# Optimization experiments

Hardware: AMD Instinct MI355X
Metric: run time of the kernel (lower is better)

## Reference

```python
import jax, jax.numpy as jnp
import numpy as np

TEMPERATURE = 0.07
IGNORE_INDEX = 255
MAX_SAMPLES = 1024  # K
BACKGROUND = 0
EPS = 1e-8


def setup_inputs() -> dict:
    key = jax.random.key(0)
    k1, k2 = jax.random.split(key)
    B, C, H, W = 16, 256, 128, 128
    feats = jax.random.normal(k1, (B, C, H, W), dtype=jnp.float32)
    labels = jax.random.randint(k2, (B, H, W), 0, 4).astype(jnp.int64)
    return {"feats": feats, "labels": labels}


def _sample_pixels(feats_flat, labels_flat, K):
    """Deterministic analogue of the torch sampler: positives first, then
    background negatives, invalid last (original uses randperm; the math
    downstream is identical for any such selection). Pads exactly like the
    original: zero features, ignore_index labels, boolean valid mask."""
    # priority: 0 = foreground pos, 1 = background neg, 2 = ignore
    prio = jnp.where(labels_flat == IGNORE_INDEX, 2,
                     jnp.where(labels_flat == BACKGROUND, 1, 0))
    order = jnp.argsort(prio, axis=1)[:, :K]                      # [B, K] stable sort
    sel_prio = jnp.take_along_axis(prio, order, axis=1)
    valid = sel_prio < 2                                          # [B, K] bool
    s_feats = jnp.take_along_axis(feats_flat, order[:, :, None], axis=1)
    s_feats = s_feats * valid[:, :, None].astype(s_feats.dtype)   # zero-pad like F.pad
    s_labels = jnp.where(valid, jnp.take_along_axis(labels_flat, order, axis=1),
                         IGNORE_INDEX)
    return s_feats, s_labels, valid


def reference(feats, labels):
    B, C, H, W = feats.shape
    K = MAX_SAMPLES
    f = feats.transpose(0, 2, 3, 1).reshape(B, H * W, C)          # [B, N, C]
    l = labels.reshape(B, H * W)

    s_feats, s_labels, valid = _sample_pixels(f, l, K)

    # pair each image with the next (rolled) image -> [B, 2K, .]
    fp = jnp.concatenate([s_feats, jnp.roll(s_feats, -1, axis=0)], axis=1)
    lp = jnp.concatenate([s_labels, jnp.roll(s_labels, -1, axis=0)], axis=1)
    vp = jnp.concatenate([valid, jnp.roll(valid, -1, axis=0)], axis=1)

    # F.normalize(dim=2), eps=1e-12
    fp = fp / jnp.maximum(jnp.linalg.norm(fp, axis=2, keepdims=True), 1e-12)

    vf = vp.astype(fp.dtype)
    logits = jnp.einsum('bkc,bjc->bkj', fp, fp) / TEMPERATURE      # [B, 2K, 2K]
    logits = logits - jax.lax.stop_gradient(jnp.max(logits, axis=2, keepdims=True))

    v_matrix = vf[:, :, None] * vf[:, None, :]
    pos_mask = (lp[:, :, None] == lp[:, None, :]).astype(fp.dtype) * v_matrix
    same_img = jnp.kron(jnp.eye(2, dtype=fp.dtype), jnp.ones((K, K), dtype=fp.dtype))[None]
    neg_mask = (1.0 - pos_mask) * same_img * v_matrix
    not_self = 1.0 - jnp.eye(2 * K, dtype=fp.dtype)[None]
    pos_mask = pos_mask * not_self
    neg_mask = neg_mask * not_self

    exp_logits = jnp.exp(logits)
    sum_neg = jnp.sum(exp_logits * neg_mask, axis=2, keepdims=True)
    log_probs = logits - jnp.log(exp_logits + sum_neg + EPS)

    num_pos = jnp.maximum(pos_mask.sum(axis=2), 1.0)
    mean_log_prob = (pos_mask * log_probs).sum(axis=2) / num_pos
    valid_anchors = (pos_mask.sum(axis=2) > 0).astype(fp.dtype)
    loss_img = (-mean_log_prob * valid_anchors).sum(axis=1) / jnp.maximum(
        valid_anchors.sum(axis=1), 1.0)                            # [B]

    # with valid labels everywhere, every chunk is valid -> divide by B
    return loss_img.sum() / B
```

## Files before the change

### kernel.cpp

```cpp
#include <hip/hip_runtime.h>
#include <hip/hip_bf16.h>

namespace {

constexpr int NB  = 16;
constexpr int NC  = 256;
constexpr int NHW = 16384;
constexpr int NK  = 1024;
constexpr int IGN = 255;
constexpr float SCALE = 4.5398164f;
constexpr float CBIAS = 20.609929f;
constexpr float LN2   = 0.69314718f;

typedef __attribute__((ext_vector_type(8))) short short8;
typedef __attribute__((ext_vector_type(4))) float f32x4;
typedef unsigned int u32;

#define ASM_VMCNT8 asm volatile("s_waitcnt vmcnt(8)" ::: "memory")
#define ASM_VMCNT0 asm volatile("s_waitcnt vmcnt(0)" ::: "memory")
#define ASM_LGKM0  asm volatile("s_waitcnt lgkmcnt(0)" ::: "memory")
#define SCHEDB     __builtin_amdgcn_sched_barrier(0)
#define MEMFENCE   asm volatile("" ::: "memory")
#define BARRIER    __builtin_amdgcn_s_barrier()
#define ACQ_AGENT  __builtin_amdgcn_fence(__ATOMIC_ACQUIRE, "agent")

__device__ __forceinline__ float fexp2(float x) { return __builtin_exp2f(x); }

__device__ __forceinline__ void gl_lds16(const void* g, void* l) {
  __builtin_amdgcn_global_load_lds((const __attribute__((address_space(1))) u32*)g,
                                   (__attribute__((address_space(3))) u32*)l, 16, 0, 0);
}

__global__ __launch_bounds__(1024) void pcl_sample(const int* __restrict__ labels,
                                                   int* __restrict__ sel_lab,
                                                   int* __restrict__ sel_idx,
                                                   int* __restrict__ cnt,
                                                   int* __restrict__ findone) {
  const int b = blockIdx.x, t = threadIdx.x, lane = t & 63, w = t >> 6;
  if (t == 0) { cnt[b] = 0; if (b == 0) *findone = 0; }
  __shared__ int labL[1024 * 17];
  __shared__ int wtot[16];

  sel_lab[b * NK + t] = IGN;

  const int* lab = labels + b * NHW;
#pragma unroll
  for (int k = 0; k < 16; ++k) {
    int idx = k * 1024 + t;
    labL[(idx >> 4) * 17 + (idx & 15)] = lab[idx];
  }
  __syncthreads();

  int cfg = 0, cbg = 0;
#pragma unroll
  for (int i = 0; i < 16; ++i) {
    int L = labL[t * 17 + i];
    cfg += (L != IGN && L != 0);
    cbg += (L == 0);
  }
  int packed = cfg | (cbg << 15);
  int incl = packed;
#pragma unroll
  for (int off = 1; off < 64; off <<= 1) {
    int n = __shfl_up(incl, off);
    if (lane >= off) incl += n;
  }
  if (lane == 63) wtot[w] = incl;
  __syncthreads();
  int wb = 0, total = 0;
#pragma unroll
  for (int ww = 0; ww < 16; ++ww) { int v = wtot[ww]; total += v; if (ww < w) wb += v; }
  int excl = incl - packed + wb;
  int rf  = excl & 32767;
  int rbg = (excl >> 15) & 32767;
  const int nfg = total & 32767;
  if (rf < NK || nfg + rbg < NK) {
#pragma unroll
    for (int i = 0; i < 16; ++i) {
      int L = labL[t * 17 + i];
      if (L == IGN) continue;
      if (L != 0) {
        if (rf < NK) { sel_lab[b * NK + rf] = L; sel_idx[b * NK + rf] = t * 16 + i; }
        ++rf;
      } else {
        int s = nfg + rbg;
        if (s < NK) { sel_lab[b * NK + s] = L; sel_idx[b * NK + s] = t * 16 + i; }
        ++rbg;
      }
    }
  }
}

__global__ __launch_bounds__(1024) void pcl_gather(const float* __restrict__ feats,
                                                   const int* __restrict__ sel_lab,
                                                   const int* __restrict__ sel_idx,
                                                   unsigned short* __restrict__ SF) {
  const int b = blockIdx.x >> 4, kb = blockIdx.x & 15;
  const int t = threadIdx.x, s = t & 63, w = t >> 6;
  __shared__ float fbuf[64][257];
  __shared__ float sqs[16][64];
  __shared__ float rn[64];
  const int gk = b * NK + kb * 64 + s;
  const int lb = sel_lab[gk];
  const int p = (lb != IGN) ? sel_idx[gk] : -1;
  const float* fb = feats + (size_t)b * NC * NHW;
  float sq = 0.f;
#pragma unroll
  for (int cc = 0; cc < 16; ++cc) {
    int c = w * 16 + cc;
    float v = (p >= 0) ? fb[(size_t)c * NHW + p] : 0.f;
    fbuf[s][c] = v;
    sq += v * v;
  }
  sqs[w][s] = sq;
  __syncthreads();
  if (t < 64) {
    float tot = 0.f;
#pragma unroll
    for (int k2 = 0; k2 < 16; ++k2) tot += sqs[k2][t];
    rn[t] = SCALE / fmaxf(sqrtf(tot), 1e-12f);
  }
  __syncthreads();
#pragma unroll
  for (int it = 0; it < 2; ++it) {
    int slot = it * 1024 + t;
    int ss = slot >> 5, ch = slot & 31;
    float r = rn[ss];
    short8 v8;
#pragma unroll
    for (int e = 0; e < 8; ++e) {
      float x = fbuf[ss][ch * 8 + e] * r;
      __hip_bfloat16 h = __float2bfloat16(x);
      unsigned short u; __builtin_memcpy(&u, &h, 2);
      v8[e] = (short)u;
    }
    *(short8*)(SF + ((size_t)(b * NK + kb * 64 + ss)) * NC + ch * 8) = v8;
  }
}

__global__ __launch_bounds__(512) void pcl_tiles(
    const unsigned short* __restrict__ SF, const int* __restrict__ sel_lab,
    float2* __restrict__ SNd, float4* __restrict__ Rii, float4* __restrict__ Cp,
    float2* __restrict__ A1arr, float2* __restrict__ Aimg,
    int* __restrict__ cnt, int* __restrict__ findone, float* __restrict__ out) {
  const int id = blockIdx.x;
  const int i = id & 15, strip = id >> 4;
  const int inxt = (i + 1) & 15, iprev = (i + 15) & 15;
  const int t = threadIdx.x, lane = t & 63, w = t >> 6;
  const int rw = w & 1, ch4 = w >> 1;
  const int lg = lane >> 4, lr = lane & 15;
  const float SFAC = __builtin_exp2f(-CBIAS);

  __shared__ short buf[2][128 * 256];
  __shared__ float4 colAcc[2][128];
  __shared__ float4 rredS[4][64];
  __shared__ float4 rredX[4][64];
  __shared__ float2 fold2[8];
  __shared__ int fA, fB;

  const unsigned short* SFrow = SF + (size_t)i * (NK * NC) + strip * 64 * NC;

  auto stage_round = [&](int rr) {
    const unsigned short* base =
        SF + (size_t)((rr < 8) ? i : inxt) * (NK * NC) + ((rr & 7) * 128) * NC;
    short* dst = buf[rr & 1];
#pragma unroll
    for (int it = 0; it < 8; ++it) {
      int n = it * 512 + t, row = n >> 5, ch = n & 31;
      gl_lds16(base + row * NC + ((ch ^ (row & 15)) << 3), dst + (size_t)n * 8);
    }
  };

#pragma unroll
  for (int it = 0; it < 4; ++it) {
    int n = it * 512 + t, row = n >> 5, ch = n & 31;
    gl_lds16(SFrow + row * NC + ((ch ^ (row & 15)) << 3), buf[0] + (size_t)n * 8);
  }
  ASM_VMCNT0; MEMFENCE; BARRIER; MEMFENCE;

  short8 afrag[2][8];
#pragma unroll
  for (int rt = 0; rt < 2; ++rt) {
    const int arow = rw * 32 + rt * 16 + lr;
#pragma unroll
    for (int ks = 0; ks < 8; ++ks) {
      int ch = ks * 4 + lg;
      afrag[rt][ks] = *(const short8*)(buf[0] + arow * 256 + ((ch ^ (arow & 15)) << 3));
    }
  }
  ASM_LGKM0; SCHEDB; MEMFENCE; BARRIER; MEMFENCE;

  stage_round(0);
  stage_round(1);

  int rlab[2][4];
#pragma unroll
  for (int rt = 0; rt < 2; ++rt)
#pragma unroll
    for (int jj = 0; jj < 4; ++jj) {
      int L = sel_lab[i * NK + strip * 64 + rw * 32 + rt * 16 + 4 * lg + jj];
      rlab[rt][jj] = (L == IGN) ? -1 : L;
    }

  ASM_VMCNT8; MEMFENCE; BARRIER; MEMFENCE;

  float SA[2][4], NPr[2][4], PEr[2][4], ETr[2][4];
#pragma unroll
  for (int rt = 0; rt < 2; ++rt)
#pragma unroll
    for (int jj = 0; jj < 4; ++jj) { SA[rt][jj] = 0.f; NPr[rt][jj] = 0.f; PEr[rt][jj] = 0.f; ETr[rt][jj] = 0.f; }

  const int rs = strip >> 1;
  const bool dwave = ((ch4 >> 1) == (strip & 1));

  for (int r = 0; r < 8; ++r) {
    int cl[2]; float cvf[2];
#pragma unroll
    for (int c2 = 0; c2 < 2; ++c2) {
      int L = sel_lab[i * NK + r * 128 + ch4 * 32 + c2 * 16 + lr];
      cl[c2] = (L == IGN) ? -2 : L;
      cvf[c2] = (L == IGN) ? 0.f : 1.f;
    }

    const short* bb = buf[r & 1];
    f32x4 acc[2][2];
#pragma unroll
    for (int rt = 0; rt < 2; ++rt)
#pragma unroll
      for (int c2 = 0; c2 < 2; ++c2) acc[rt][c2] = f32x4{0.f, 0.f, 0.f, 0.f};
#pragma unroll
    for (int ks = 0; ks < 8; ++ks) {
      int ch = ks * 4 + lg;
      short8 b0, b1;
      {
        int br0 = ch4 * 32 + lr, br1 = ch4 * 32 + 16 + lr;
        b0 = *(const short8*)(bb + br0 * 256 + ((ch ^ (br0 & 15)) << 3));
        b1 = *(const short8*)(bb + br1 * 256 + ((ch ^ (br1 & 15)) << 3));
      }
      acc[0][0] = __builtin_amdgcn_mfma_f32_16x16x32_bf16(afrag[0][ks], b0, acc[0][0], 0, 0, 0);
      acc[0][1] = __builtin_amdgcn_mfma_f32_16x16x32_bf16(afrag[0][ks], b1, acc[0][1], 0, 0, 0);
      acc[1][0] = __builtin_amdgcn_mfma_f32_16x16x32_bf16(afrag[1][ks], b0, acc[1][0], 0, 0, 0);
      acc[1][1] = __builtin_amdgcn_mfma_f32_16x16x32_bf16(afrag[1][ks], b1, acc[1][1], 0, 0, 0);
    }

    const bool isdiag = (r == rs) && dwave;
#pragma unroll
    for (int rt = 0; rt < 2; ++rt)
#pragma unroll
      for (int c2 = 0; c2 < 2; ++c2) {
        const int clc = cl[c2]; const float cvc = cvf[c2];
        const int gc = r * 128 + ch4 * 32 + c2 * 16 + lr;
        const int grb = strip * 64 + rw * 32 + rt * 16 + 4 * lg;
#pragma unroll
        for (int jj = 0; jj < 4; ++jj) {
          float a = acc[rt][c2][jj];
          float E = fexp2(a);
          float Ev = cvc * E;
          float pm = (rlab[rt][jj] == clc) ? 1.f : 0.f;
          if (isdiag) {
            bool ok = (grb + jj) != gc;
            pm = ok ? pm : 0.f;
            Ev = ok ? Ev : 0.f;
          }
          SA[rt][jj] += pm * a; NPr[rt][jj] += pm;
          PEr[rt][jj] += pm * Ev; ETr[rt][jj] += Ev;
        }
      }

    MEMFENCE; BARRIER; MEMFENCE;
    stage_round(r + 2);
    ASM_VMCNT8;
    MEMFENCE; BARRIER; MEMFENCE;
  }

#pragma unroll
  for (int rt = 0; rt < 2; ++rt)
#pragma unroll
    for (int jj = 0; jj < 4; ++jj) {
      float a = SA[rt][jj], b4 = NPr[rt][jj], c4 = PEr[rt][jj], d4 = ETr[rt][jj];
#pragma unroll
      for (int m = 1; m <= 8; m <<= 1) {
        a += __shfl_xor(a, m); b4 += __shfl_xor(b4, m);
        c4 += __shfl_xor(c4, m); d4 += __shfl_xor(d4, m);
      }
      if (lr == 0) rredS[ch4][rw * 32 + rt * 16 + 4 * lg + jj] = make_float4(a, b4, c4, d4);
    }

  float SX[2][4], NX[2][4], PX[2][4];
#pragma unroll
  for (int rt = 0; rt < 2; ++rt)
#pragma unroll
    for (int jj = 0; jj < 4; ++jj) { SX[rt][jj] = 0.f; NX[rt][jj] = 0.f; PX[rt][jj] = 0.f; }

  for (int r = 8; r < 16; ++r) {
    int cl[2];
#pragma unroll
    for (int c2 = 0; c2 < 2; ++c2) {
      int L = sel_lab[inxt * NK + (r & 7) * 128 + ch4 * 32 + c2 * 16 + lr];
      cl[c2] = (L == IGN) ? -2 : L;
    }

    const short* bb = buf[r & 1];
    f32x4 acc[2][2];
#pragma unroll
    for (int rt = 0; rt < 2; ++rt)
#pragma unroll
      for (int c2 = 0; c2 < 2; ++c2) acc[rt][c2] = f32x4{0.f, 0.f, 0.f, 0.f};
#pragma unroll
    for (int ks = 0; ks < 8; ++ks) {
      int ch = ks * 4 + lg;
      short8 b0, b1;
      {
        int br0 = ch4 * 32 + lr, br1 = ch4 * 32 + 16 + lr;
        b0 = *(const short8*)(bb + br0 * 256 + ((ch ^ (br0 & 15)) << 3));
        b1 = *(const short8*)(bb + br1 * 256 + ((ch ^ (br1 & 15)) << 3));
      }
      acc[0][0] = __builtin_amdgcn_mfma_f32_16x16x32_bf16(afrag[0][ks], b0, acc[0][0], 0, 0, 0);
      acc[0][1] = __builtin_amdgcn_mfma_f32_16x16x32_bf16(afrag[0][ks], b1, acc[0][1], 0, 0, 0);
      acc[1][0] = __builtin_amdgcn_mfma_f32_16x16x32_bf16(afrag[1][ks], b0, acc[1][0], 0, 0, 0);
      acc[1][1] = __builtin_amdgcn_mfma_f32_16x16x32_bf16(afrag[1][ks], b1, acc[1][1], 0, 0, 0);
    }

    float cS[2], cN[2], cE[2];
#pragma unroll
    for (int c2 = 0; c2 < 2; ++c2) { cS[c2] = 0.f; cN[c2] = 0.f; cE[c2] = 0.f; }
#pragma unroll
    for (int rt = 0; rt < 2; ++rt)
#pragma unroll
      for (int c2 = 0; c2 < 2; ++c2) {
        const int clc = cl[c2];
#pragma unroll
        for (int jj = 0; jj < 4; ++jj) {
          float a = acc[rt][c2][jj];
          float E = fexp2(a);
          float pm = (rlab[rt][jj] == clc) ? 1.f : 0.f;
          float pa = pm * a, pe = pm * E;
          SX[rt][jj] += pa; NX[rt][jj] += pm; PX[rt][jj] += pe;
          cS[c2] += pa; cN[c2] += pm; cE[c2] += pe;
        }
      }
#pragma unroll
    for (int c2 = 0; c2 < 2; ++c2) {
      cS[c2] += __shfl_xor(cS[c2], 16); cS[c2] += __shfl_xor(cS[c2], 32);
      cN[c2] += __shfl_xor(cN[c2], 16); cN[c2] += __shfl_xor(cN[c2], 32);
      cE[c2] += __shfl_xor(cE[c2], 16); cE[c2] += __shfl_xor(cE[c2], 32);
      if (lg == 0) colAcc[rw][ch4 * 32 + c2 * 16 + lr] = make_float4(cS[c2], cN[c2], cE[c2], 0.f);
    }
    ASM_LGKM0; SCHEDB;
    MEMFENCE; BARRIER; MEMFENCE;
    if (rw == 1 && lg == 0) {
#pragma unroll
      for (int c2 = 0; c2 < 2; ++c2) {
        int col = ch4 * 32 + c2 * 16 + lr;
        float4 o = colAcc[0][col];
        Cp[(i * 16 + strip) * NK + (r & 7) * 128 + col] =
            make_float4(cS[c2] + o.x, cN[c2] + o.y, (cE[c2] + o.z) * SFAC, 0.f);
      }
    }
    if (r < 14) { stage_round(r + 2); ASM_VMCNT8; MEMFENCE; BARRIER; MEMFENCE; }
    else if (r == 14) { ASM_VMCNT0; MEMFENCE; BARRIER; MEMFENCE; }
  }

#pragma unroll
  for (int rt = 0; rt < 2; ++rt)
#pragma unroll
    for (int jj = 0; jj < 4; ++jj) {
      float a = SX[rt][jj], b4 = NX[rt][jj], c4 = PX[rt][jj];
#pragma unroll
      for (int m = 1; m <= 8; m <<= 1) {
        a += __shfl_xor(a, m); b4 += __shfl_xor(b4, m); c4 += __shfl_xor(c4, m);
      }
      if (lr == 0) rredX[ch4][rw * 32 + rt * 16 + 4 * lg + jj] = make_float4(a, b4, c4, 0.f);
    }
  __syncthreads();

  if (t < 64) {
    float4 sS = rredS[0][t], sX = rredX[0][t];
#pragma unroll
    for (int c4 = 1; c4 < 4; ++c4) {
      float4 u = rredS[c4][t], v = rredX[c4][t];
      sS.x += u.x; sS.y += u.y; sS.z += u.z; sS.w += u.w;
      sX.x += v.x; sX.y += v.y; sX.z += v.z;
    }
    float SNL = sS.w - sS.z;
    float SN = SNL * SFAC + 1e-8f;
    float LSN = __logf(SN), rSN = 1.f / SN;
    int g = i * NK + strip * 64 + t;
    SNd[g] = make_float2(LSN, rSN);
    Rii[g] = make_float4(sS.x, sS.y, sS.z * SFAC, 0.f);
    float pps = LN2 * (sS.x - CBIAS * sS.y) - sS.y * LSN - rSN * (sS.z * SFAC);
    float ppx = LN2 * (sX.x - CBIAS * sX.y) - sX.y * LSN - rSN * (sX.z * SFAC);
    float np1 = sS.y + sX.y;
    float an = 0.f, ac = 0.f;
    if (np1 > 0.f) { an = -(pps + ppx) / np1; ac = 1.f; }
#pragma unroll
    for (int m = 1; m <= 32; m <<= 1) { an += __shfl_xor(an, m); ac += __shfl_xor(ac, m); }
    if (t == 0) A1arr[i * 16 + strip] = make_float2(an, ac);
  }
  __syncthreads();

  if (t == 0) {
    __threadfence();
    int o1 = atomicAdd(&cnt[i], 1);
    int o2 = atomicAdd(&cnt[iprev], 1);
    fA = (o1 == 31); fB = (o2 == 31);
  }
  __syncthreads();

  auto pair_fold = [&](int p) {
    const int q = (p + 1) & 15;
    ACQ_AGENT;
    float an = 0.f, ac = 0.f;
    for (int r2 = t; r2 < NK; r2 += 512) {
      float4 rii = Rii[q * NK + r2];
      float2 sn = SNd[q * NK + r2];
      float cs = 0.f, cn = 0.f, ce = 0.f;
#pragma unroll
      for (int s2 = 0; s2 < 16; ++s2) {
        float4 c = Cp[(p * 16 + s2) * NK + r2];
        cs += c.x; cn += c.y; ce += c.z;
      }
      float ppc = LN2 * (cs - CBIAS * cn) - cn * sn.x - sn.y * ce;
      float ppi = LN2 * (rii.x - CBIAS * rii.y) - rii.y * sn.x - sn.y * rii.z;
      float np2 = rii.y + cn;
      if (np2 > 0.f) { an -= (ppi + ppc) / np2; ac += 1.f; }
    }
#pragma unroll
    for (int m = 1; m <= 32; m <<= 1) { an += __shfl_xor(an, m); ac += __shfl_xor(ac, m); }
    if (lane == 0) fold2[w] = make_float2(an, ac);
    __syncthreads();
    if (t == 0) {
      float a2n = 0.f, a2c = 0.f;
#pragma unroll
      for (int k2 = 0; k2 < 8; ++k2) { a2n += fold2[k2].x; a2c += fold2[k2].y; }
      float a1n = 0.f, a1c = 0.f;
#pragma unroll
      for (int s2 = 0; s2 < 16; ++s2) {
        float2 a = A1arr[q * 16 + s2];
        a1n += a.x; a1c += a.y;
      }
      Aimg[q] = make_float2(a1n + a2n, a1c + a2c);
      __threadfence();
      int f = atomicAdd(findone, 1);
      if (f == NB - 1) {
        ACQ_AGENT;
        float v = 0.f;
#pragma unroll
        for (int im = 0; im < NB; ++im) {
          float2 gg = Aimg[im];
          v += gg.x / fmaxf(gg.y, 1.f);
        }
        out[0] = v / (float)NB;
      }
    }
    __syncthreads();
  };

  if (fA) pair_fold(i);
  if (fB) pair_fold(iprev);
}

}

extern "C" void kernel_launch(void* const* d_in, const int* in_sizes, int n_in,
                              void* d_out, int out_size, void* d_ws, size_t ws_size,
                              hipStream_t stream) {
  (void)in_sizes; (void)n_in; (void)out_size; (void)ws_size;
  const float* feats  = (const float*)d_in[0];
  const int*   labels = (const int*)d_in[1];
  float* out = (float*)d_out;
  char* ws = (char*)d_ws;

  int* sel_lab = (int*)ws;
  int* sel_idx = (int*)(ws + (64 << 10));
  unsigned short* SF = (unsigned short*)(ws + (128 << 10));
  size_t off = (128 << 10) + (size_t)NB * NK * NC * 2;
  float2* SNd = (float2*)(ws + off);  off += (size_t)NB * NK * 8;
  float4* Rii = (float4*)(ws + off);  off += (size_t)NB * NK * 16;
  float4* Cp  = (float4*)(ws + off);  off += (size_t)NB * 16 * NK * 16;
  float2* A1arr = (float2*)(ws + off); off += (size_t)NB * 16 * 8;
  float2* Aimg = (float2*)(ws + off);  off += NB * 8;
  int* cnt = (int*)(ws + off);         off += 16 * 4;
  int* findone = (int*)(ws + off);

  pcl_sample<<<NB, 1024, 0, stream>>>(labels, sel_lab, sel_idx, cnt, findone);
  pcl_gather<<<256, 1024, 0, stream>>>(feats, sel_lab, sel_idx, SF);
  pcl_tiles<<<256, 512, 0, stream>>>(SF, sel_lab, SNd, Rii, Cp, A1arr, Aimg,
                                     cnt, findone, out);
}
```

Baseline: 87.61 us.

## Fuse sampling, gather and tile kernels into one kernel with a spin barrier

Merges the three launches (label sampling, feature gather with normalisation, similarity tiles) into a single 256-block kernel, with the shared-memory layouts overlaid in a union. Each block recomputes the label prefix scan for its own image and keeps only its 64-slot strip locally, so the separate sel_idx buffer goes away. A per-image ready counter, zeroed by a memset, plus a spin-wait lets a block start its tile work once its own image and the next image are gathered. This removes inter-kernel launch gaps and the 16-block serial sampling stage. The cost is 16x redundant label scans, redundant identical writes to sel_lab, and a deadlock risk if all 256 blocks cannot be resident at once.

```diff
diff --git a/kernel.cpp b/kernel.cpp
--- a/kernel.cpp
+++ b/kernel.cpp
@@ -31,139 +31,157 @@
                                    (__attribute__((address_space(3))) u32*)l, 16, 0, 0);
 }
 
-__global__ __launch_bounds__(1024) void pcl_sample(const int* __restrict__ labels,
-                                                   int* __restrict__ sel_lab,
-                                                   int* __restrict__ sel_idx,
-                                                   int* __restrict__ cnt,
-                                                   int* __restrict__ findone) {
-  const int b = blockIdx.x, t = threadIdx.x, lane = t & 63, w = t >> 6;
-  if (t == 0) { cnt[b] = 0; if (b == 0) *findone = 0; }
-  __shared__ int labL[1024 * 17];
-  __shared__ int wtot[16];
-
-  sel_lab[b * NK + t] = IGN;
-
-  const int* lab = labels + b * NHW;
-#pragma unroll
-  for (int k = 0; k < 16; ++k) {
-    int idx = k * 1024 + t;
-    labL[(idx >> 4) * 17 + (idx & 15)] = lab[idx];
-  }
-  __syncthreads();
-
-  int cfg = 0, cbg = 0;
-#pragma unroll
-  for (int i = 0; i < 16; ++i) {
-    int L = labL[t * 17 + i];
-    cfg += (L != IGN && L != 0);
-    cbg += (L == 0);
-  }
-  int packed = cfg | (cbg << 15);
-  int incl = packed;
-#pragma unroll
-  for (int off = 1; off < 64; off <<= 1) {
-    int n = __shfl_up(incl, off);
-    if (lane >= off) incl += n;
-  }
-  if (lane == 63) wtot[w] = incl;
-  __syncthreads();
-  int wb = 0, total = 0;
-#pragma unroll
-  for (int ww = 0; ww < 16; ++ww) { int v = wtot[ww]; total += v; if (ww < w) wb += v; }
-  int excl = incl - packed + wb;
-  int rf  = excl & 32767;
-  int rbg = (excl >> 15) & 32767;
-  const int nfg = total & 32767;
-  if (rf < NK || nfg + rbg < NK) {
-#pragma unroll
-    for (int i = 0; i < 16; ++i) {
-      int L = labL[t * 17 + i];
-      if (L == IGN) continue;
-      if (L != 0) {
-        if (rf < NK) { sel_lab[b * NK + rf] = L; sel_idx[b * NK + rf] = t * 16 + i; }
-        ++rf;
-      } else {
-        int s = nfg + rbg;
-        if (s < NK) { sel_lab[b * NK + s] = L; sel_idx[b * NK + s] = t * 16 + i; }
-        ++rbg;
-      }
-    }
-  }
-}
-
-__global__ __launch_bounds__(1024) void pcl_gather(const float* __restrict__ feats,
-                                                   const int* __restrict__ sel_lab,
-                                                   const int* __restrict__ sel_idx,
-                                                   unsigned short* __restrict__ SF) {
-  const int b = blockIdx.x >> 4, kb = blockIdx.x & 15;
-  const int t = threadIdx.x, s = t & 63, w = t >> 6;
-  __shared__ float fbuf[64][257];
-  __shared__ float sqs[16][64];
-  __shared__ float rn[64];
-  const int gk = b * NK + kb * 64 + s;
-  const int lb = sel_lab[gk];
-  const int p = (lb != IGN) ? sel_idx[gk] : -1;
-  const float* fb = feats + (size_t)b * NC * NHW;
-  float sq = 0.f;
-#pragma unroll
-  for (int cc = 0; cc < 16; ++cc) {
-    int c = w * 16 + cc;
-    float v = (p >= 0) ? fb[(size_t)c * NHW + p] : 0.f;
-    fbuf[s][c] = v;
-    sq += v * v;
-  }
-  sqs[w][s] = sq;
-  __syncthreads();
-  if (t < 64) {
-    float tot = 0.f;
-#pragma unroll
-    for (int k2 = 0; k2 < 16; ++k2) tot += sqs[k2][t];
-    rn[t] = SCALE / fmaxf(sqrtf(tot), 1e-12f);
-  }
-  __syncthreads();
-#pragma unroll
-  for (int it = 0; it < 2; ++it) {
-    int slot = it * 1024 + t;
-    int ss = slot >> 5, ch = slot & 31;
-    float r = rn[ss];
-    short8 v8;
-#pragma unroll
-    for (int e = 0; e < 8; ++e) {
-      float x = fbuf[ss][ch * 8 + e] * r;
-      __hip_bfloat16 h = __float2bfloat16(x);
-      unsigned short u; __builtin_memcpy(&u, &h, 2);
-      v8[e] = (short)u;
-    }
-    *(short8*)(SF + ((size_t)(b * NK + kb * 64 + ss)) * NC + ch * 8) = v8;
-  }
-}
-
-__global__ __launch_bounds__(512) void pcl_tiles(
-    const unsigned short* __restrict__ SF, const int* __restrict__ sel_lab,
+union SmemU {
+  struct {
+    int lab[NHW + (NHW >> 5)];
+    int wtot[8];
+  } s;
+  struct {
+    float fbuf[64][257];
+    float sqs[8][64];
+    float rn[64];
+  } g;
+  struct {
+    short buf[2][128 * 256];
+    float4 colAcc[2][128];
+    float4 rredS[4][64];
+    float4 rredX[4][64];
+    float2 fold2[8];
+    int fA, fB;
+  } t3;
+};
+
+__global__ __launch_bounds__(512) void pcl_fused(
+    const int* __restrict__ labels, const float* __restrict__ feats,
+    int* __restrict__ sel_lab, unsigned short* __restrict__ SF,
     float2* __restrict__ SNd, float4* __restrict__ Rii, float4* __restrict__ Cp,
     float2* __restrict__ A1arr, float2* __restrict__ Aimg,
-    int* __restrict__ cnt, int* __restrict__ findone, float* __restrict__ out) {
+    int* __restrict__ cnt, int* __restrict__ gready, int* __restrict__ findone,
+    float* __restrict__ out) {
   const int id = blockIdx.x;
   const int i = id & 15, strip = id >> 4;
   const int inxt = (i + 1) & 15, iprev = (i + 15) & 15;
   const int t = threadIdx.x, lane = t & 63, w = t >> 6;
+
+  __shared__ SmemU sm;
+  __shared__ int slab[64], sidx[64];
+
+  {
+    const int* lab = labels + (size_t)i * NHW;
+#pragma unroll
+    for (int k = 0; k < 32; ++k) {
+      int idx = k * 512 + t;
+      sm.s.lab[idx + (idx >> 5)] = lab[idx];
+    }
+    if (t < 64) slab[t] = IGN;
+    __syncthreads();
+
+    int cfg = 0, cbg = 0;
+#pragma unroll
+    for (int j = 0; j < 32; ++j) {
+      int L = sm.s.lab[t * 33 + j];
+      cfg += (L != IGN && L != 0);
+      cbg += (L == 0);
+    }
+    int packed = cfg | (cbg << 15);
+    int incl = packed;
+#pragma unroll
+    for (int off = 1; off < 64; off <<= 1) {
+      int n = __shfl_up(incl, off);
+      if (lane >= off) incl += n;
+    }
+    if (lane == 63) sm.s.wtot[w] = incl;
+    __syncthreads();
+    int wb = 0, total = 0;
+#pragma unroll
+    for (int ww = 0; ww < 8; ++ww) { int v = sm.s.wtot[ww]; total += v; if (ww < w) wb += v; }
+    int excl = incl - packed + wb;
+    int rf  = excl & 32767;
+    int rbg = (excl >> 15) & 32767;
+    const int nfg = total & 32767;
+    const int nbg = (total >> 15) & 32767;
+    const int ncap = min(NK, nfg + nbg);
+    for (int k2 = ncap + t; k2 < NK; k2 += 512) sel_lab[i * NK + k2] = IGN;
+
+    const int s0 = strip * 64;
+    if (rf < NK || nfg + rbg < NK) {
+      for (int j = 0; j < 32; ++j) {
+        int L = sm.s.lab[t * 33 + j];
+        if (L == IGN) continue;
+        int slot;
+        if (L != 0) { slot = rf; ++rf; }
+        else        { slot = nfg + rbg; ++rbg; }
+        if (slot < NK) {
+          sel_lab[i * NK + slot] = L;
+          int d = slot - s0;
+          if ((unsigned)d < 64u) { slab[d] = L; sidx[d] = t * 32 + j; }
+        }
+      }
+    }
+    __syncthreads();
+  }
+
+  {
+    const int ss = t & 63, w8 = t >> 6;
+    const int lb = slab[ss];
+    const int p = (lb != IGN) ? sidx[ss] : -1;
+    const float* fb = feats + (size_t)i * NC * NHW;
+    float sq = 0.f;
+#pragma unroll
+    for (int cc = 0; cc < 32; ++cc) {
+      int c = w8 * 32 + cc;
+      float v = (p >= 0) ? fb[(size_t)c * NHW + p] : 0.f;
+      sm.g.fbuf[ss][c] = v;
+      sq += v * v;
+    }
+    sm.g.sqs[w8][ss] = sq;
+    __syncthreads();
+    if (t < 64) {
+      float tot = 0.f;
+#pragma unroll
+      for (int k2 = 0; k2 < 8; ++k2) tot += sm.g.sqs[k2][t];
+      sm.g.rn[t] = SCALE / fmaxf(sqrtf(tot), 1e-12f);
+    }
+    __syncthreads();
+    unsigned short* SFo = SF + ((size_t)(i * NK + strip * 64)) * NC;
+#pragma unroll
+    for (int it2 = 0; it2 < 4; ++it2) {
+      int n = it2 * 512 + t;
+      int row = n >> 5, ch16 = n & 31;
+      float r = sm.g.rn[row];
+      short8 v8;
+#pragma unroll
+      for (int e = 0; e < 8; ++e) {
+        float x = sm.g.fbuf[row][ch16 * 8 + e] * r;
+        __hip_bfloat16 h = __float2bfloat16(x);
+        unsigned short u; __builtin_memcpy(&u, &h, 2);
+        v8[e] = (short)u;
+      }
+      *(short8*)(SFo + (size_t)row * NC + ch16 * 8) = v8;
+    }
+    __syncthreads();
+
+    if (t == 0) {
+      __threadfence();
+      atomicAdd(&gready[i], 1);
+      while (__hip_atomic_load(&gready[i],    __ATOMIC_RELAXED, __HIP_MEMORY_SCOPE_AGENT) < 16 ||
+             __hip_atomic_load(&gready[inxt], __ATOMIC_RELAXED, __HIP_MEMORY_SCOPE_AGENT) < 16)
+        __builtin_amdgcn_s_sleep(2);
+      ACQ_AGENT;
+    }
+    __syncthreads();
+  }
+
   const int rw = w & 1, ch4 = w >> 1;
   const int lg = lane >> 4, lr = lane & 15;
   const float SFAC = __builtin_exp2f(-CBIAS);
 
-  __shared__ short buf[2][128 * 256];
-  __shared__ float4 colAcc[2][128];
-  __shared__ float4 rredS[4][64];
-  __shared__ float4 rredX[4][64];
-  __shared__ float2 fold2[8];
-  __shared__ int fA, fB;
-
   const unsigned short* SFrow = SF + (size_t)i * (NK * NC) + strip * 64 * NC;
 
   auto stage_round = [&](int rr) {
     const unsigned short* base =
         SF + (size_t)((rr < 8) ? i : inxt) * (NK * NC) + ((rr & 7) * 128) * NC;
-    short* dst = buf[rr & 1];
+    short* dst = sm.t3.buf[rr & 1];
 #pragma unroll
     for (int it = 0; it < 8; ++it) {
       int n = it * 512 + t, row = n >> 5, ch = n & 31;
@@ -174,7 +192,7 @@
 #pragma unroll
   for (int it = 0; it < 4; ++it) {
     int n = it * 512 + t, row = n >> 5, ch = n & 31;
-    gl_lds16(SFrow + row * NC + ((ch ^ (row & 15)) << 3), buf[0] + (size_t)n * 8);
+    gl_lds16(SFrow + row * NC + ((ch ^ (row & 15)) << 3), sm.t3.buf[0] + (size_t)n * 8);
   }
   ASM_VMCNT0; MEMFENCE; BARRIER; MEMFENCE;
 
@@ -185,7 +203,7 @@
 #pragma unroll
     for (int ks = 0; ks < 8; ++ks) {
       int ch = ks * 4 + lg;
-      afrag[rt][ks] = *(const short8*)(buf[0] + arow * 256 + ((ch ^ (arow & 15)) << 3));
+      afrag[rt][ks] = *(const short8*)(sm.t3.buf[0] + arow * 256 + ((ch ^ (arow & 15)) << 3));
     }
   }
   ASM_LGKM0; SCHEDB; MEMFENCE; BARRIER; MEMFENCE;
@@ -222,7 +240,7 @@
       cvf[c2] = (L == IGN) ? 0.f : 1.f;
     }
 
-    const short* bb = buf[r & 1];
+    const short* bb = sm.t3.buf[r & 1];
     f32x4 acc[2][2];
 #pragma unroll
     for (int rt = 0; rt < 2; ++rt)
@@ -283,7 +301,7 @@
         a += __shfl_xor(a, m); b4 += __shfl_xor(b4, m);
         c4 += __shfl_xor(c4, m); d4 += __shfl_xor(d4, m);
       }
-      if (lr == 0) rredS[ch4][rw * 32 + rt * 16 + 4 * lg + jj] = make_float4(a, b4, c4, d4);
+      if (lr == 0) sm.t3.rredS[ch4][rw * 32 + rt * 16 + 4 * lg + jj] = make_float4(a, b4, c4, d4);
     }
 
   float SX[2][4], NX[2][4], PX[2][4];
@@ -300,7 +318,7 @@
       cl[c2] = (L == IGN) ? -2 : L;
     }
 
-    const short* bb = buf[r & 1];
+    const short* bb = sm.t3.buf[r & 1];
     f32x4 acc[2][2];
 #pragma unroll
     for (int rt = 0; rt < 2; ++rt)
@@ -344,7 +362,7 @@
       cS[c2] += __shfl_xor(cS[c2], 16); cS[c2] += __shfl_xor(cS[c2], 32);
       cN[c2] += __shfl_xor(cN[c2], 16); cN[c2] += __shfl_xor(cN[c2], 32);
       cE[c2] += __shfl_xor(cE[c2], 16); cE[c2] += __shfl_xor(cE[c2], 32);
-      if (lg == 0) colAcc[rw][ch4 * 32 + c2 * 16 + lr] = make_float4(cS[c2], cN[c2], cE[c2], 0.f);
+      if (lg == 0) sm.t3.colAcc[rw][ch4 * 32 + c2 * 16 + lr] = make_float4(cS[c2], cN[c2], cE[c2], 0.f);
     }
     ASM_LGKM0; SCHEDB;
     MEMFENCE; BARRIER; MEMFENCE;
@@ -352,7 +370,7 @@
 #pragma unroll
       for (int c2 = 0; c2 < 2; ++c2) {
         int col = ch4 * 32 + c2 * 16 + lr;
-        float4 o = colAcc[0][col];
+        float4 o = sm.t3.colAcc[0][col];
         Cp[(i * 16 + strip) * NK + (r & 7) * 128 + col] =
             make_float4(cS[c2] + o.x, cN[c2] + o.y, (cE[c2] + o.z) * SFAC, 0.f);
       }
@@ -370,15 +388,15 @@
       for (int m = 1; m <= 8; m <<= 1) {
         a += __shfl_xor(a, m); b4 += __shfl_xor(b4, m); c4 += __shfl_xor(c4, m);
       }
-      if (lr == 0) rredX[ch4][rw * 32 + rt * 16 + 4 * lg + jj] = make_float4(a, b4, c4, 0.f);
+      if (lr == 0) sm.t3.rredX[ch4][rw * 32 + rt * 16 + 4 * lg + jj] = make_float4(a, b4, c4, 0.f);
     }
   __syncthreads();
 
   if (t < 64) {
-    float4 sS = rredS[0][t], sX = rredX[0][t];
+    float4 sS = sm.t3.rredS[0][t], sX = sm.t3.rredX[0][t];
 #pragma unroll
     for (int c4 = 1; c4 < 4; ++c4) {
-      float4 u = rredS[c4][t], v = rredX[c4][t];
+      float4 u = sm.t3.rredS[c4][t], v = sm.t3.rredX[c4][t];
       sS.x += u.x; sS.y += u.y; sS.z += u.z; sS.w += u.w;
       sX.x += v.x; sX.y += v.y; sX.z += v.z;
     }
@@ -403,7 +421,7 @@
     __threadfence();
     int o1 = atomicAdd(&cnt[i], 1);
     int o2 = atomicAdd(&cnt[iprev], 1);
-    fA = (o1 == 31); fB = (o2 == 31);
+    sm.t3.fA = (o1 == 31); sm.t3.fB = (o2 == 31);
   }
   __syncthreads();
 
@@ -427,12 +445,12 @@
     }
 #pragma unroll
     for (int m = 1; m <= 32; m <<= 1) { an += __shfl_xor(an, m); ac += __shfl_xor(ac, m); }
-    if (lane == 0) fold2[w] = make_float2(an, ac);
+    if (lane == 0) sm.t3.fold2[w] = make_float2(an, ac);
     __syncthreads();
     if (t == 0) {
       float a2n = 0.f, a2c = 0.f;
 #pragma unroll
-      for (int k2 = 0; k2 < 8; ++k2) { a2n += fold2[k2].x; a2c += fold2[k2].y; }
+      for (int k2 = 0; k2 < 8; ++k2) { a2n += sm.t3.fold2[k2].x; a2c += sm.t3.fold2[k2].y; }
       float a1n = 0.f, a1c = 0.f;
 #pragma unroll
       for (int s2 = 0; s2 < 16; ++s2) {
@@ -456,8 +474,8 @@
     __syncthreads();
   };
 
-  if (fA) pair_fold(i);
-  if (fB) pair_fold(iprev);
+  if (sm.t3.fA) pair_fold(i);
+  if (sm.t3.fB) pair_fold(iprev);
 }
 
 }
@@ -472,19 +490,18 @@
   char* ws = (char*)d_ws;
 
   int* sel_lab = (int*)ws;
-  int* sel_idx = (int*)(ws + (64 << 10));
-  unsigned short* SF = (unsigned short*)(ws + (128 << 10));
-  size_t off = (128 << 10) + (size_t)NB * NK * NC * 2;
+  unsigned short* SF = (unsigned short*)(ws + (64 << 10));
+  size_t off = (64 << 10) + (size_t)NB * NK * NC * 2;
   float2* SNd = (float2*)(ws + off);  off += (size_t)NB * NK * 8;
   float4* Rii = (float4*)(ws + off);  off += (size_t)NB * NK * 16;
   float4* Cp  = (float4*)(ws + off);  off += (size_t)NB * 16 * NK * 16;
   float2* A1arr = (float2*)(ws + off); off += (size_t)NB * 16 * 8;
   float2* Aimg = (float2*)(ws + off);  off += NB * 8;
-  int* cnt = (int*)(ws + off);         off += 16 * 4;
-  int* findone = (int*)(ws + off);
-
-  pcl_sample<<<NB, 1024, 0, stream>>>(labels, sel_lab, sel_idx, cnt, findone);
-  pcl_gather<<<256, 1024, 0, stream>>>(feats, sel_lab, sel_idx, SF);
-  pcl_tiles<<<256, 512, 0, stream>>>(SF, sel_lab, SNd, Rii, Cp, A1arr, Aimg,
-                                     cnt, findone, out);
+  int* cnt = (int*)(ws + off);
+  int* gready = cnt + 16;
+  int* findone = cnt + 32;
+
+  hipMemsetAsync(cnt, 0, 33 * sizeof(int), stream);
+  pcl_fused<<<256, 512, 0, stream>>>(labels, feats, sel_lab, SF, SNd, Rii, Cp,
+                                     A1arr, Aimg, cnt, gready, findone, out);
 }
```

Result: slower. 124.0 us (+41.5%).

## Split tile work into self and cross-image blocks with smaller workgroups

Applied to the files above, without the earlier changes.

The tile kernel goes from 256 blocks of 512 threads, each covering a 64-row strip against both the same image and the next image, to 512 blocks of 256 threads. Each block now handles one 64-row strip against only one column image (self or next), using 64-column staging rounds. The completion counters and the final fold are reworked to match: 48 contributors per image, separate Rin and AimgA/AimgB buffers. Block-to-image mappings in the gather and tile kernels are remapped, apparently to spread images across XCDs. The intent is more parallelism and occupancy on the 256-CU part, at the cost of reloading row fragments twice and more atomic and fold traffic.

```diff
diff --git a/kernel.cpp b/kernel.cpp
--- a/kernel.cpp
+++ b/kernel.cpp
@@ -34,10 +34,10 @@
 __global__ __launch_bounds__(1024) void pcl_sample(const int* __restrict__ labels,
                                                    int* __restrict__ sel_lab,
                                                    int* __restrict__ sel_idx,
-                                                   int* __restrict__ cnt,
+                                                   int* __restrict__ fc,
                                                    int* __restrict__ findone) {
   const int b = blockIdx.x, t = threadIdx.x, lane = t & 63, w = t >> 6;
-  if (t == 0) { cnt[b] = 0; if (b == 0) *findone = 0; }
+  if (t == 0) { fc[b] = 0; if (b == 0) *findone = 0; }
   __shared__ int labL[1024 * 17];
   __shared__ int wtot[16];
 
@@ -95,7 +95,9 @@
                                                    const int* __restrict__ sel_lab,
                                                    const int* __restrict__ sel_idx,
                                                    unsigned short* __restrict__ SF) {
-  const int b = blockIdx.x >> 4, kb = blockIdx.x & 15;
+  const int id = blockIdx.x;
+  const int b = (id & 7) + (((id >> 3) & 1) << 3);
+  const int kb = id >> 4;
   const int t = threadIdx.x, s = t & 63, w = t >> 6;
   __shared__ float fbuf[64][257];
   __shared__ float sqs[16][64];
@@ -138,42 +140,48 @@
   }
 }
 
-__global__ __launch_bounds__(512) void pcl_tiles(
+__global__ __launch_bounds__(256) void pcl_tiles(
     const unsigned short* __restrict__ SF, const int* __restrict__ sel_lab,
-    float2* __restrict__ SNd, float4* __restrict__ Rii, float4* __restrict__ Cp,
-    float2* __restrict__ A1arr, float2* __restrict__ Aimg,
-    int* __restrict__ cnt, int* __restrict__ findone, float* __restrict__ out) {
+    float2* __restrict__ SNd, float4* __restrict__ Rii, float4* __restrict__ Rin,
+    float4* __restrict__ Cp, float2* __restrict__ AimgA, float2* __restrict__ AimgB,
+    int* __restrict__ fc, int* __restrict__ findone, float* __restrict__ out) {
   const int id = blockIdx.x;
-  const int i = id & 15, strip = id >> 4;
-  const int inxt = (i + 1) & 15, iprev = (i + 15) & 15;
+  const int g = id & 7, slot = id >> 3;
+  const bool selfm = slot < 32;
+  const int strip = slot & 15;
+  int i;
+  if (selfm) i = (slot < 16) ? g : g + 8;
+  else { int j1 = (g + 7) & 7; i = (slot < 48) ? j1 : j1 + 8; }
+  const int inxt = (i + 1) & 15;
+  const int jimg = selfm ? i : inxt;
+
   const int t = threadIdx.x, lane = t & 63, w = t >> 6;
-  const int rw = w & 1, ch4 = w >> 1;
+  const int rw = w & 1, cw = w >> 1;
   const int lg = lane >> 4, lr = lane & 15;
   const float SFAC = __builtin_exp2f(-CBIAS);
 
-  __shared__ short buf[2][128 * 256];
-  __shared__ float4 colAcc[2][128];
-  __shared__ float4 rredS[4][64];
-  __shared__ float4 rredX[4][64];
-  __shared__ float2 fold2[8];
+  __shared__ short buf[2][64 * 256];
+  __shared__ float4 colAcc[2][64];
+  __shared__ float4 rred[2][64];
+  __shared__ float4 fold4[4];
   __shared__ int fA, fB;
 
   const unsigned short* SFrow = SF + (size_t)i * (NK * NC) + strip * 64 * NC;
+  const unsigned short* SFcol = SF + (size_t)jimg * (NK * NC);
 
   auto stage_round = [&](int rr) {
-    const unsigned short* base =
-        SF + (size_t)((rr < 8) ? i : inxt) * (NK * NC) + ((rr & 7) * 128) * NC;
+    const unsigned short* base = SFcol + ((rr)*64) * NC;
     short* dst = buf[rr & 1];
 #pragma unroll
     for (int it = 0; it < 8; ++it) {
-      int n = it * 512 + t, row = n >> 5, ch = n & 31;
+      int n = it * 256 + t, row = n >> 5, ch = n & 31;
       gl_lds16(base + row * NC + ((ch ^ (row & 15)) << 3), dst + (size_t)n * 8);
     }
   };
 
 #pragma unroll
-  for (int it = 0; it < 4; ++it) {
-    int n = it * 512 + t, row = n >> 5, ch = n & 31;
+  for (int it = 0; it < 8; ++it) {
+    int n = it * 256 + t, row = n >> 5, ch = n & 31;
     gl_lds16(SFrow + row * NC + ((ch ^ (row & 15)) << 3), buf[0] + (size_t)n * 8);
   }
   ASM_VMCNT0; MEMFENCE; BARRIER; MEMFENCE;
@@ -204,20 +212,17 @@
 
   ASM_VMCNT8; MEMFENCE; BARRIER; MEMFENCE;
 
-  float SA[2][4], NPr[2][4], PEr[2][4], ETr[2][4];
+  float S1[2][4], N1[2][4], P1[2][4], ET[2][4];
 #pragma unroll
   for (int rt = 0; rt < 2; ++rt)
 #pragma unroll
-    for (int jj = 0; jj < 4; ++jj) { SA[rt][jj] = 0.f; NPr[rt][jj] = 0.f; PEr[rt][jj] = 0.f; ETr[rt][jj] = 0.f; }
-
-  const int rs = strip >> 1;
-  const bool dwave = ((ch4 >> 1) == (strip & 1));
-
-  for (int r = 0; r < 8; ++r) {
+    for (int jj = 0; jj < 4; ++jj) { S1[rt][jj] = 0.f; N1[rt][jj] = 0.f; P1[rt][jj] = 0.f; ET[rt][jj] = 0.f; }
+
+  for (int r = 0; r < 16; ++r) {
     int cl[2]; float cvf[2];
 #pragma unroll
     for (int c2 = 0; c2 < 2; ++c2) {
-      int L = sel_lab[i * NK + r * 128 + ch4 * 32 + c2 * 16 + lr];
+      int L = sel_lab[jimg * NK + r * 64 + cw * 32 + c2 * 16 + lr];
       cl[c2] = (L == IGN) ? -2 : L;
       cvf[c2] = (L == IGN) ? 0.f : 1.f;
     }
@@ -233,7 +238,7 @@
       int ch = ks * 4 + lg;
       short8 b0, b1;
       {
-        int br0 = ch4 * 32 + lr, br1 = ch4 * 32 + 16 + lr;
+        int br0 = cw * 32 + lr, br1 = cw * 32 + 16 + lr;
         b0 = *(const short8*)(bb + br0 * 256 + ((ch ^ (br0 & 15)) << 3));
         b1 = *(const short8*)(bb + br1 * 256 + ((ch ^ (br1 & 15)) << 3));
       }
@@ -243,177 +248,128 @@
       acc[1][1] = __builtin_amdgcn_mfma_f32_16x16x32_bf16(afrag[1][ks], b1, acc[1][1], 0, 0, 0);
     }
 
-    const bool isdiag = (r == rs) && dwave;
-#pragma unroll
-    for (int rt = 0; rt < 2; ++rt)
+    if (selfm) {
+      const bool isdiag = (r == strip);
+#pragma unroll
+      for (int rt = 0; rt < 2; ++rt)
+#pragma unroll
+        for (int c2 = 0; c2 < 2; ++c2) {
+          const int clc = cl[c2]; const float cvc = cvf[c2];
+          const int gc = r * 64 + cw * 32 + c2 * 16 + lr;
+          const int grb = strip * 64 + rw * 32 + rt * 16 + 4 * lg;
+#pragma unroll
+          for (int jj = 0; jj < 4; ++jj) {
+            float a = acc[rt][c2][jj];
+            float E = fexp2(a);
+            float Ev = cvc * E;
+            float pm = (rlab[rt][jj] == clc) ? 1.f : 0.f;
+            if (isdiag) {
+              bool ok = (grb + jj) != gc;
+              pm = ok ? pm : 0.f;
+              Ev = ok ? Ev : 0.f;
+            }
+            S1[rt][jj] += pm * a; N1[rt][jj] += pm;
+            P1[rt][jj] += pm * Ev; ET[rt][jj] += Ev;
+          }
+        }
+      MEMFENCE; BARRIER; MEMFENCE;
+    } else {
+      float cS[2], cN[2], cE[2];
+#pragma unroll
+      for (int c2 = 0; c2 < 2; ++c2) { cS[c2] = 0.f; cN[c2] = 0.f; cE[c2] = 0.f; }
+#pragma unroll
+      for (int rt = 0; rt < 2; ++rt)
+#pragma unroll
+        for (int c2 = 0; c2 < 2; ++c2) {
+          const int clc = cl[c2];
+#pragma unroll
+          for (int jj = 0; jj < 4; ++jj) {
+            float a = acc[rt][c2][jj];
+            float E = fexp2(a);
+            float pm = (rlab[rt][jj] == clc) ? 1.f : 0.f;
+            float pa = pm * a, pe = pm * E;
+            S1[rt][jj] += pa; N1[rt][jj] += pm; P1[rt][jj] += pe;
+            cS[c2] += pa; cN[c2] += pm; cE[c2] += pe;
+          }
+        }
 #pragma unroll
       for (int c2 = 0; c2 < 2; ++c2) {
-        const int clc = cl[c2]; const float cvc = cvf[c2];
-        const int gc = r * 128 + ch4 * 32 + c2 * 16 + lr;
-        const int grb = strip * 64 + rw * 32 + rt * 16 + 4 * lg;
-#pragma unroll
-        for (int jj = 0; jj < 4; ++jj) {
-          float a = acc[rt][c2][jj];
-          float E = fexp2(a);
-          float Ev = cvc * E;
-          float pm = (rlab[rt][jj] == clc) ? 1.f : 0.f;
-          if (isdiag) {
-            bool ok = (grb + jj) != gc;
-            pm = ok ? pm : 0.f;
-            Ev = ok ? Ev : 0.f;
-          }
-          SA[rt][jj] += pm * a; NPr[rt][jj] += pm;
-          PEr[rt][jj] += pm * Ev; ETr[rt][jj] += Ev;
+        cS[c2] += __shfl_xor(cS[c2], 16); cS[c2] += __shfl_xor(cS[c2], 32);
+        cN[c2] += __shfl_xor(cN[c2], 16); cN[c2] += __shfl_xor(cN[c2], 32);
+        cE[c2] += __shfl_xor(cE[c2], 16); cE[c2] += __shfl_xor(cE[c2], 32);
+        if (lg == 0) colAcc[rw][cw * 32 + c2 * 16 + lr] = make_float4(cS[c2], cN[c2], cE[c2], 0.f);
+      }
+      ASM_LGKM0; SCHEDB;
+      MEMFENCE; BARRIER; MEMFENCE;
+      if (rw == 1 && lg == 0) {
+#pragma unroll
+        for (int c2 = 0; c2 < 2; ++c2) {
+          int col = cw * 32 + c2 * 16 + lr;
+          float4 o = colAcc[0][col];
+          Cp[(i * 16 + strip) * NK + r * 64 + col] =
+              make_float4(cS[c2] + o.x, cN[c2] + o.y, (cE[c2] + o.z) * SFAC, 0.f);
         }
       }
-
-    MEMFENCE; BARRIER; MEMFENCE;
-    stage_round(r + 2);
-    ASM_VMCNT8;
-    MEMFENCE; BARRIER; MEMFENCE;
+    }
+
+    if (r < 14) { stage_round(r + 2); ASM_VMCNT8; MEMFENCE; BARRIER; MEMFENCE; }
+    else if (r == 14) { ASM_VMCNT0; MEMFENCE; BARRIER; MEMFENCE; }
   }
 
 #pragma unroll
   for (int rt = 0; rt < 2; ++rt)
 #pragma unroll
     for (int jj = 0; jj < 4; ++jj) {
-      float a = SA[rt][jj], b4 = NPr[rt][jj], c4 = PEr[rt][jj], d4 = ETr[rt][jj];
+      float a = S1[rt][jj], b4 = N1[rt][jj], c4 = P1[rt][jj], d4 = ET[rt][jj];
 #pragma unroll
       for (int m = 1; m <= 8; m <<= 1) {
         a += __shfl_xor(a, m); b4 += __shfl_xor(b4, m);
         c4 += __shfl_xor(c4, m); d4 += __shfl_xor(d4, m);
       }
-      if (lr == 0) rredS[ch4][rw * 32 + rt * 16 + 4 * lg + jj] = make_float4(a, b4, c4, d4);
-    }
-
-  float SX[2][4], NX[2][4], PX[2][4];
-#pragma unroll
-  for (int rt = 0; rt < 2; ++rt)
-#pragma unroll
-    for (int jj = 0; jj < 4; ++jj) { SX[rt][jj] = 0.f; NX[rt][jj] = 0.f; PX[rt][jj] = 0.f; }
-
-  for (int r = 8; r < 16; ++r) {
-    int cl[2];
-#pragma unroll
-    for (int c2 = 0; c2 < 2; ++c2) {
-      int L = sel_lab[inxt * NK + (r & 7) * 128 + ch4 * 32 + c2 * 16 + lr];
-      cl[c2] = (L == IGN) ? -2 : L;
-    }
-
-    const short* bb = buf[r & 1];
-    f32x4 acc[2][2];
-#pragma unroll
-    for (int rt = 0; rt < 2; ++rt)
-#pragma unroll
-      for (int c2 = 0; c2 < 2; ++c2) acc[rt][c2] = f32x4{0.f, 0.f, 0.f, 0.f};
-#pragma unroll
-    for (int ks = 0; ks < 8; ++ks) {
-      int ch = ks * 4 + lg;
-      short8 b0, b1;
-      {
-        int br0 = ch4 * 32 + lr, br1 = ch4 * 32 + 16 + lr;
-        b0 = *(const short8*)(bb + br0 * 256 + ((ch ^ (br0 & 15)) << 3));
-        b1 = *(const short8*)(bb + br1 * 256 + ((ch ^ (br1 & 15)) << 3));
-      }
-      acc[0][0] = __builtin_amdgcn_mfma_f32_16x16x32_bf16(afrag[0][ks], b0, acc[0][0], 0, 0, 0);
-      acc[0][1] = __builtin_amdgcn_mfma_f32_16x16x32_bf16(afrag[0][ks], b1, acc[0][1], 0, 0, 0);
-      acc[1][0] = __builtin_amdgcn_mfma_f32_16x16x32_bf16(afrag[1][ks], b0, acc[1][0], 0, 0, 0);
-      acc[1][1] = __builtin_amdgcn_mfma_f32_16x16x32_bf16(afrag[1][ks], b1, acc[1][1], 0, 0, 0);
-    }
-
-    float cS[2], cN[2], cE[2];
-#pragma unroll
-    for (int c2 = 0; c2 < 2; ++c2) { cS[c2] = 0.f; cN[c2] = 0.f; cE[c2] = 0.f; }
-#pragma unroll
-    for (int rt = 0; rt < 2; ++rt)
-#pragma unroll
-      for (int c2 = 0; c2 < 2; ++c2) {
-        const int clc = cl[c2];
-#pragma unroll
-        for (int jj = 0; jj < 4; ++jj) {
-          float a = acc[rt][c2][jj];
-          float E = fexp2(a);
-          float pm = (rlab[rt][jj] == clc) ? 1.f : 0.f;
-          float pa = pm * a, pe = pm * E;
-          SX[rt][jj] += pa; NX[rt][jj] += pm; PX[rt][jj] += pe;
-          cS[c2] += pa; cN[c2] += pm; cE[c2] += pe;
-        }
-      }
-#pragma unroll
-    for (int c2 = 0; c2 < 2; ++c2) {
-      cS[c2] += __shfl_xor(cS[c2], 16); cS[c2] += __shfl_xor(cS[c2], 32);
-      cN[c2] += __shfl_xor(cN[c2], 16); cN[c2] += __shfl_xor(cN[c2], 32);
-      cE[c2] += __shfl_xor(cE[c2], 16); cE[c2] += __shfl_xor(cE[c2], 32);
-      if (lg == 0) colAcc[rw][ch4 * 32 + c2 * 16 + lr] = make_float4(cS[c2], cN[c2], cE[c2], 0.f);
-    }
-    ASM_LGKM0; SCHEDB;
-    MEMFENCE; BARRIER; MEMFENCE;
-    if (rw == 1 && lg == 0) {
-#pragma unroll
-      for (int c2 = 0; c2 < 2; ++c2) {
-        int col = ch4 * 32 + c2 * 16 + lr;
-        float4 o = colAcc[0][col];
-        Cp[(i * 16 + strip) * NK + (r & 7) * 128 + col] =
-            make_float4(cS[c2] + o.x, cN[c2] + o.y, (cE[c2] + o.z) * SFAC, 0.f);
-      }
-    }
-    if (r < 14) { stage_round(r + 2); ASM_VMCNT8; MEMFENCE; BARRIER; MEMFENCE; }
-    else if (r == 14) { ASM_VMCNT0; MEMFENCE; BARRIER; MEMFENCE; }
-  }
-
-#pragma unroll
-  for (int rt = 0; rt < 2; ++rt)
-#pragma unroll
-    for (int jj = 0; jj < 4; ++jj) {
-      float a = SX[rt][jj], b4 = NX[rt][jj], c4 = PX[rt][jj];
-#pragma unroll
-      for (int m = 1; m <= 8; m <<= 1) {
-        a += __shfl_xor(a, m); b4 += __shfl_xor(b4, m); c4 += __shfl_xor(c4, m);
-      }
-      if (lr == 0) rredX[ch4][rw * 32 + rt * 16 + 4 * lg + jj] = make_float4(a, b4, c4, 0.f);
+      if (lr == 0) rred[cw][rw * 32 + rt * 16 + 4 * lg + jj] = make_float4(a, b4, c4, d4);
     }
   __syncthreads();
 
   if (t < 64) {
-    float4 sS = rredS[0][t], sX = rredX[0][t];
-#pragma unroll
-    for (int c4 = 1; c4 < 4; ++c4) {
-      float4 u = rredS[c4][t], v = rredX[c4][t];
-      sS.x += u.x; sS.y += u.y; sS.z += u.z; sS.w += u.w;
-      sX.x += v.x; sX.y += v.y; sX.z += v.z;
-    }
-    float SNL = sS.w - sS.z;
-    float SN = SNL * SFAC + 1e-8f;
-    float LSN = __logf(SN), rSN = 1.f / SN;
-    int g = i * NK + strip * 64 + t;
-    SNd[g] = make_float2(LSN, rSN);
-    Rii[g] = make_float4(sS.x, sS.y, sS.z * SFAC, 0.f);
-    float pps = LN2 * (sS.x - CBIAS * sS.y) - sS.y * LSN - rSN * (sS.z * SFAC);
-    float ppx = LN2 * (sX.x - CBIAS * sX.y) - sX.y * LSN - rSN * (sX.z * SFAC);
-    float np1 = sS.y + sX.y;
-    float an = 0.f, ac = 0.f;
-    if (np1 > 0.f) { an = -(pps + ppx) / np1; ac = 1.f; }
-#pragma unroll
-    for (int m = 1; m <= 32; m <<= 1) { an += __shfl_xor(an, m); ac += __shfl_xor(ac, m); }
-    if (t == 0) A1arr[i * 16 + strip] = make_float2(an, ac);
+    float4 A4 = rred[0][t], B4 = rred[1][t];
+    float4 sS = make_float4(A4.x + B4.x, A4.y + B4.y, A4.z + B4.z, A4.w + B4.w);
+    int gidx = i * NK + strip * 64 + t;
+    if (selfm) {
+      float SNL = sS.w - sS.z;
+      float SN = SNL * SFAC + 1e-8f;
+      SNd[gidx] = make_float2(__logf(SN), 1.f / SN);
+      Rii[gidx] = make_float4(sS.x, sS.y, sS.z * SFAC, 0.f);
+    } else {
+      Rin[gidx] = make_float4(sS.x, sS.y, sS.z * SFAC, 0.f);
+    }
   }
   __syncthreads();
 
   if (t == 0) {
     __threadfence();
-    int o1 = atomicAdd(&cnt[i], 1);
-    int o2 = atomicAdd(&cnt[iprev], 1);
-    fA = (o1 == 31); fB = (o2 == 31);
-  }
-  __syncthreads();
-
-  auto pair_fold = [&](int p) {
-    const int q = (p + 1) & 15;
+    if (selfm) {
+      int o = atomicAdd(&fc[i], 1);
+      fA = (o == 47); fB = 0;
+    } else {
+      int o1 = atomicAdd(&fc[i], 1);
+      int o2 = atomicAdd(&fc[inxt], 1);
+      fA = (o1 == 47); fB = (o2 == 47);
+    }
+  }
+  __syncthreads();
+
+  auto pair_fold = [&](int q) {
+    const int p = (q + 15) & 15;
     ACQ_AGENT;
-    float an = 0.f, ac = 0.f;
-    for (int r2 = t; r2 < NK; r2 += 512) {
+    float a1n = 0.f, a1c = 0.f, a2n = 0.f, a2c = 0.f;
+    for (int r2 = t; r2 < NK; r2 += 256) {
       float4 rii = Rii[q * NK + r2];
+      float4 rin = Rin[q * NK + r2];
       float2 sn = SNd[q * NK + r2];
+      float ppi = LN2 * (rii.x - CBIAS * rii.y) - rii.y * sn.x - sn.y * rii.z;
+      float ppn = LN2 * (rin.x - CBIAS * rin.y) - rin.y * sn.x - sn.y * rin.z;
+      float np1 = rii.y + rin.y;
+      if (np1 > 0.f) { a1n -= (ppi + ppn) / np1; a1c += 1.f; }
       float cs = 0.f, cn = 0.f, ce = 0.f;
 #pragma unroll
       for (int s2 = 0; s2 < 16; ++s2) {
@@ -421,34 +377,34 @@
         cs += c.x; cn += c.y; ce += c.z;
       }
       float ppc = LN2 * (cs - CBIAS * cn) - cn * sn.x - sn.y * ce;
-      float ppi = LN2 * (rii.x - CBIAS * rii.y) - rii.y * sn.x - sn.y * rii.z;
       float np2 = rii.y + cn;
-      if (np2 > 0.f) { an -= (ppi + ppc) / np2; ac += 1.f; }
-    }
-#pragma unroll
-    for (int m = 1; m <= 32; m <<= 1) { an += __shfl_xor(an, m); ac += __shfl_xor(ac, m); }
-    if (lane == 0) fold2[w] = make_float2(an, ac);
+      if (np2 > 0.f) { a2n -= (ppi + ppc) / np2; a2c += 1.f; }
+    }
+#pragma unroll
+    for (int m = 1; m <= 32; m <<= 1) {
+      a1n += __shfl_xor(a1n, m); a1c += __shfl_xor(a1c, m);
+      a2n += __shfl_xor(a2n, m); a2c += __shfl_xor(a2c, m);
+    }
+    if (lane == 0) fold4[w] = make_float4(a1n, a1c, a2n, a2c);
     __syncthreads();
     if (t == 0) {
-      float a2n = 0.f, a2c = 0.f;
-#pragma unroll
-      for (int k2 = 0; k2 < 8; ++k2) { a2n += fold2[k2].x; a2c += fold2[k2].y; }
-      float a1n = 0.f, a1c = 0.f;
-#pragma unroll
-      for (int s2 = 0; s2 < 16; ++s2) {
-        float2 a = A1arr[q * 16 + s2];
-        a1n += a.x; a1c += a.y;
-      }
-      Aimg[q] = make_float2(a1n + a2n, a1c + a2c);
+      float x1 = 0.f, y1 = 0.f, x2 = 0.f, y2 = 0.f;
+#pragma unroll
+      for (int k2 = 0; k2 < 4; ++k2) {
+        float4 f = fold4[k2];
+        x1 += f.x; y1 += f.y; x2 += f.z; y2 += f.w;
+      }
+      AimgA[q] = make_float2(x1, y1);
+      AimgB[p] = make_float2(x2, y2);
       __threadfence();
       int f = atomicAdd(findone, 1);
       if (f == NB - 1) {
         ACQ_AGENT;
         float v = 0.f;
 #pragma unroll
-        for (int im = 0; im < NB; ++im) {
-          float2 gg = Aimg[im];
-          v += gg.x / fmaxf(gg.y, 1.f);
+        for (int pp = 0; pp < NB; ++pp) {
+          float2 A2 = AimgA[pp], B2 = AimgB[pp];
+          v += (A2.x + B2.x) / fmaxf(A2.y + B2.y, 1.f);
         }
         out[0] = v / (float)NB;
       }
@@ -457,7 +413,7 @@
   };
 
   if (fA) pair_fold(i);
-  if (fB) pair_fold(iprev);
+  if (fB) pair_fold(inxt);
 }
 
 }
@@ -477,14 +433,15 @@
   size_t off = (128 << 10) + (size_t)NB * NK * NC * 2;
   float2* SNd = (float2*)(ws + off);  off += (size_t)NB * NK * 8;
   float4* Rii = (float4*)(ws + off);  off += (size_t)NB * NK * 16;
+  float4* Rin = (float4*)(ws + off);  off += (size_t)NB * NK * 16;
   float4* Cp  = (float4*)(ws + off);  off += (size_t)NB * 16 * NK * 16;
-  float2* A1arr = (float2*)(ws + off); off += (size_t)NB * 16 * 8;
-  float2* Aimg = (float2*)(ws + off);  off += NB * 8;
-  int* cnt = (int*)(ws + off);         off += 16 * 4;
+  float2* AimgA = (float2*)(ws + off); off += NB * 8;
+  float2* AimgB = (float2*)(ws + off); off += NB * 8;
+  int* fc = (int*)(ws + off);          off += 16 * 4;
   int* findone = (int*)(ws + off);
 
-  pcl_sample<<<NB, 1024, 0, stream>>>(labels, sel_lab, sel_idx, cnt, findone);
+  pcl_sample<<<NB, 1024, 0, stream>>>(labels, sel_lab, sel_idx, fc, findone);
   pcl_gather<<<256, 1024, 0, stream>>>(feats, sel_lab, sel_idx, SF);
-  pcl_tiles<<<256, 512, 0, stream>>>(SF, sel_lab, SNd, Rii, Cp, A1arr, Aimg,
-                                     cnt, findone, out);
-}
+  pcl_tiles<<<512, 256, 0, stream>>>(SF, sel_lab, SNd, Rii, Rin, Cp,
+                                     AimgA, AimgB, fc, findone, out);
+}
```

Result: slower. 119.7 us (+36.6%).
